# Optimization experiments

Measured on AMD Instinct MI355X. Metric: run time of the kernel, lower is better.

## Reference

```python
import jax, jax.numpy as jnp
import numpy as np

T, D, N, K, V = 4, 1024, 256, 64, 32000
SGLD_A, SGLD_B, SGLD_C = 0.01, 1.0, 0.55
PHI_VAR, ETA_VAR = 1.0, 1.0
ZERO = 1e-6

def jax_exp(x):
    return jnp.clip(jnp.exp(jnp.clip(x, -700.0, 700.0)), ZERO)

def setup_inputs() -> dict:
    key = jax.random.key(0)
    ks = jax.random.split(key, 13)
    W = jax.random.randint(ks[0], (T, D, N), 0, V, dtype=jnp.int32)
    Z = jax.random.randint(ks[1], (T, D, N), 0, K - 1, dtype=jnp.int32)
    prop_word_idx = jax.random.randint(ks[2], (T, D, N), 0, N, dtype=jnp.int32)
    prop_topic = jax.random.randint(ks[3], (T, D, N), 0, K - 1, dtype=jnp.int32)
    u_mh = jax.random.uniform(ks[4], (T, D, N, 2), dtype=jnp.float32)
    noise_eta = jax.random.normal(ks[5], (T, D), dtype=jnp.float32)
    noise_phi = jax.random.normal(ks[6], (T,), dtype=jnp.float32)
    alpha = jax.random.normal(ks[7], (T, K), dtype=jnp.float32)
    phi = jax.random.normal(ks[8], (T, V, K), dtype=jnp.float32) * 0.1
    eta = jax.random.normal(ks[9], (T, D, K), dtype=jnp.float32) * 0.1
    CDK = jax.random.uniform(ks[10], (T, D, K), dtype=jnp.float32) * (N / K)
    CWK = jax.random.uniform(ks[11], (T, V, K), dtype=jnp.float32)
    CK = jax.random.uniform(ks[12], (T, K), dtype=jnp.float32) * (D * N / K)
    return dict(W=W, Z=Z, prop_word_idx=prop_word_idx, prop_topic=prop_topic,
                u_mh=u_mh, noise_eta=noise_eta, noise_phi=noise_phi,
                alpha=alpha, phi=phi, eta=eta, CDK=CDK, CWK=CWK, CK=CK)

def reference(W, Z, prop_word_idx, prop_topic, u_mh, noise_eta, noise_phi,
              alpha, phi, eta, CDK, CWK, CK):
    eps = SGLD_A * (SGLD_B + 0.0) ** (-SGLD_C)  # SGLD step at iteration 0

    # --- SGLD update of eta (per doc), vmapped over (T, D) via broadcasting ---
    prior_eta = (alpha[:, None, :] - eta) / ETA_VAR                 # [T,D,K]
    grad_eta = CDK - N * jax.nn.softmax(eta, axis=-1)               # [T,D,K]
    eta_new = eta + eps / 2 * (grad_eta + prior_eta) + noise_eta[..., None] * eps

    tt = jnp.arange(T)[:, None, None]   # [T,1,1]
    dd = jnp.arange(D)[None, :, None]   # [1,D,1]

    # --- MH step 1: word-proposal (acceptance via phi ratio) ---
    pre = Z                                                           # [T,D,N]
    prop1 = jnp.take_along_axis(Z, prop_word_idx, axis=2)             # [T,D,N]
    a1 = jax_exp(phi[tt, W, prop1]) / jax_exp(phi[tt, W, pre])
    k1 = jnp.where(u_mh[..., 0] < a1, prop1, pre)

    # --- MH step 2: topic-proposal (acceptance via eta ratio) ---
    a2 = jax_exp(eta_new[tt, dd, prop_topic]) / jax_exp(eta_new[tt, dd, k1])
    z_new = jnp.where(u_mh[..., 1] < a2, prop_topic, k1)              # [T,D,N]

    # --- scatter counter updates (add new assignment, remove old) ---
    CDK_new = CDK.at[tt, dd, z_new].add(1.0).at[tt, dd, Z].add(-1.0)
    CWK_new = CWK.at[tt, W, z_new].add(1.0).at[tt, W, Z].add(-1.0)
    CK_new = CK.at[tt, z_new].add(1.0).at[tt, Z].add(-1.0)

    # --- SGLD update of phi: sequential over T (reads updated phi[t-1]) ---
    rows = [phi[t] for t in range(T)]   # each [V,K]
    phi_sigma = 1.0 / (1.0 / 100.0 + 1.0 / PHI_VAR)
    for t in range(T):
        if t == 0:
            prior = (2.0 * phi[1] * (phi_sigma / PHI_VAR) - 2.0 * rows[0]) / PHI_VAR
        elif t == T - 1:
            prior = (rows[t - 1] - rows[t]) / PHI_VAR
        else:
            prior = (phi[t + 1] + rows[t - 1] - 2.0 * rows[t]) / PHI_VAR
        grad = CWK_new[t] - CK_new[t][None, :] * jax.nn.softmax(rows[t], axis=0)
        rows[t] = rows[t] + eps / 2 * (grad + prior) + noise_phi[t] * eps
    phi_new = jnp.stack(rows)

    return (eta_new, phi_new, CDK_new, CWK_new, CK_new, z_new)
```

## Files before the change

kernel.cpp:

```cpp
#include <hip/hip_runtime.h>

#define T 4
#define D 1024
#define NN 256
#define K 64
#define V 32000
#define VK (V*K)
#define TD (T*D)

__device__ __forceinline__ float jexp(float x) {
    x = fminf(fmaxf(x, -700.0f), 700.0f);
    return fmaxf(expf(x), 1e-6f);
}


__global__ void phi_colsum_kernel(const float* __restrict__ phi,
                                  float* __restrict__ S_part,
                                  unsigned int* __restrict__ delta,
                                  const float* __restrict__ CK,
                                  float* __restrict__ CK_new)
{
    int blk = blockIdx.x;
    int tid = threadIdx.x;

    {
        uint4* dz = (uint4*)delta;
        int g = blk * 256 + tid;
        uint4 z4 = make_uint4(0u, 0u, 0u, 0u);
        #pragma unroll
        for (int i = 0; i < 8; ++i)
            dz[g + i * 128000] = z4;
    }
    if (blk == 0) CK_new[tid] = CK[tid];

    int t = blk / 125;
    int vbase = (blk % 125) * 256;
    int k = tid & 63;
    int r = tid >> 6;
    const float* base = phi + (size_t)t * VK;
    float s = 0.0f;
    #pragma unroll 4
    for (int it = 0; it < 64; ++it) {
        int v = vbase + it * 4 + r;
        s += expf(base[v * K + k]);
    }
    __shared__ float sm[256];
    sm[tid] = s;
    __syncthreads();
    if (tid < 64) {
        S_part[blk * 64 + tid] = sm[tid] + sm[tid + 64] +
                                 sm[tid + 128] + sm[tid + 192];
    }
}

__global__ void mh_eta_kernel(const int* __restrict__ W, const int* __restrict__ Z,
                              const int* __restrict__ pwi, const int* __restrict__ ptop,
                              const float* __restrict__ u, const float* __restrict__ phi,
                              const float* __restrict__ eta,
                              const float* __restrict__ alpha,
                              const float* __restrict__ noise_eta,
                              const float* __restrict__ CDK,
                              float* __restrict__ eta_new,
                              float* __restrict__ CDK_new,
                              unsigned int* __restrict__ plus,
                              unsigned int* __restrict__ minus,
                              float* __restrict__ z_out)
{
    int b = blockIdx.x;
    int r = ((b & 7) << 9) | (b >> 3);
    int t = r >> 10;
    int n = threadIdx.x;

    __shared__ float esh[K];
    __shared__ int   hist[K];

    int w     = W[r * NN + n];
    int pre   = Z[r * NN + n];
    int pw    = pwi[r * NN + n];
    int prop1 = Z[r * NN + pw];
    int pt    = ptop[r * NN + n];
    float2 uu = ((const float2*)u)[(size_t)r * NN + n];

    const float* prow = phi + ((size_t)t * V + w) * K;
    float f1 = prow[prop1];
    float f0 = prow[pre];

    float cdk = 0.0f;
    if (n < 64) {
        float x = eta[r * K + n];
        float m = x;
        #pragma unroll
        for (int off = 32; off >= 1; off >>= 1)
            m = fmaxf(m, __shfl_xor(m, off, 64));
        float e = expf(x - m);
        float s = e;
        #pragma unroll
        for (int off = 32; off >= 1; off >>= 1)
            s += __shfl_xor(s, off, 64);
        float smx = e / s;
        cdk = CDK[r * K + n];
        float grad  = cdk - (float)NN * smx;
        float prior = alpha[t * K + n] - x;
        float en = x + 0.005f * (grad + prior) + noise_eta[r] * 0.01f;
        esh[n] = en;
        eta_new[r * K + n] = en;
    } else if (n < 128) {
        hist[n - 64] = 0;
    }
    __syncthreads();

    float a1 = jexp(f1) / jexp(f0);
    int k1 = (uu.x < a1) ? prop1 : pre;

    float a2 = jexp(esh[pt]) / jexp(esh[k1]);
    int z = (uu.y < a2) ? pt : k1;

    atomicAdd(&hist[z], 1);
    atomicAdd(&hist[pre], -1);
    __syncthreads();

    z_out[r * NN + n] = (float)z;
    if (z != pre) {
        size_t rowbase = ((size_t)t * V + w) * 16;
        atomicAdd(&plus [rowbase + (z   >> 2)], 1u << ((z   & 3) * 8));
        atomicAdd(&minus[rowbase + (pre >> 2)], 1u << ((pre & 3) * 8));
    }
    if (n < K) {
        CDK_new[r * K + n] = cdk + (float)hist[n];
    }
}

__global__ void reduce_kernel(const float* __restrict__ S_part,
                              const float* __restrict__ CDKn,
                              const float* __restrict__ CDK,
                              float* __restrict__ S,
                              float* __restrict__ CK_new)
{
    int b = blockIdx.x;
    int tid = threadIdx.x;

    if (b < 4 && tid < 64) {
        float s = 0.0f;
        #pragma unroll 5
        for (int i = 0; i < 125; ++i)
            s += S_part[(b * 125 + i) * 64 + tid];
        S[b * 64 + tid] = s;
    }

    int t  = b >> 4;
    int k  = tid & 63;
    int dl = tid >> 6;
    int dbase = (b & 15) << 6;
    float s = 0.0f;
    #pragma unroll
    for (int i = 0; i < 16; ++i) {
        int d = dbase + dl + (i << 2);
        size_t idx = ((size_t)(t << 10) + d) * 64 + k;
        s += CDKn[idx] - CDK[idx];
    }
    __shared__ float sm[256];
    sm[tid] = s;
    __syncthreads();
    if (tid < 64) {
        float tot = sm[k] + sm[k + 64] + sm[k + 128] + sm[k + 192];
        if (tot != 0.0f) atomicAdd(&CK_new[(t << 6) + k], tot);
    }
}

__global__ void phi_update_kernel(const float* __restrict__ phi,
                                  const float* __restrict__ CWK,
                                  const unsigned int* __restrict__ plus,
                                  const unsigned int* __restrict__ minus,
                                  const float* __restrict__ CKn,
                                  const float* __restrict__ S,
                                  const float* __restrict__ noise_phi,
                                  float* __restrict__ phi_new,
                                  float* __restrict__ CWK_new)
{
    int i4 = blockIdx.x * 256 + threadIdx.x;
    int kg = i4 & 15;
    const float eps = 0.01f;
    const float half_eps = 0.005f;
    const float sig = 1.0f / 1.01f;

    const float4* phi4  = (const float4*)phi;
    const float4* cwk4  = (const float4*)CWK;
    const float4* ck4   = (const float4*)CKn;
    const float4* s4    = (const float4*)S;
    float4*       out4  = (float4*)phi_new;
    float4*       cwkn4 = (float4*)CWK_new;

    float4 p0 = phi4[i4];
    float4 p1 = phi4[i4 +     512000];
    float4 p2 = phi4[i4 + 2 * 512000];
    float4 p3 = phi4[i4 + 3 * 512000];

    float4 c0 = cwk4[i4];
    float4 c1 = cwk4[i4 +     512000];
    float4 c2 = cwk4[i4 + 2 * 512000];
    float4 c3 = cwk4[i4 + 3 * 512000];

    unsigned int pl0 = plus [i4],               mi0 = minus[i4];
    unsigned int pl1 = plus [i4 +     512000],  mi1 = minus[i4 +     512000];
    unsigned int pl2 = plus [i4 + 2 * 512000],  mi2 = minus[i4 + 2 * 512000];
    unsigned int pl3 = plus [i4 + 3 * 512000],  mi3 = minus[i4 + 3 * 512000];

    float4 ckn0 = ck4[kg],      ckn1 = ck4[16 + kg];
    float4 ckn2 = ck4[32 + kg], ckn3 = ck4[48 + kg];
    float4 ss0 = s4[kg],        ss1 = s4[16 + kg];
    float4 ss2 = s4[32 + kg],   ss3 = s4[48 + kg];

    float np0 = noise_phi[0] * eps, np1 = noise_phi[1] * eps;
    float np2 = noise_phi[2] * eps, np3 = noise_phi[3] * eps;

    float4 o0, o1, o2, o3, w0, w1, w2, w3;
    #pragma unroll
    for (int j = 0; j < 4; ++j) {
        int sh = j * 8;
        float q0 = (&p0.x)[j], q1 = (&p1.x)[j], q2 = (&p2.x)[j], q3 = (&p3.x)[j];
        float d0 = (float)((pl0 >> sh) & 255u) - (float)((mi0 >> sh) & 255u);
        float d1 = (float)((pl1 >> sh) & 255u) - (float)((mi1 >> sh) & 255u);
        float d2 = (float)((pl2 >> sh) & 255u) - (float)((mi2 >> sh) & 255u);
        float d3 = (float)((pl3 >> sh) & 255u) - (float)((mi3 >> sh) & 255u);
        float cw0 = (&c0.x)[j] + d0;
        float cw1 = (&c1.x)[j] + d1;
        float cw2 = (&c2.x)[j] + d2;
        float cw3 = (&c3.x)[j] + d3;
        (&w0.x)[j] = cw0; (&w1.x)[j] = cw1; (&w2.x)[j] = cw2; (&w3.x)[j] = cw3;

        float g0 = cw0 - (&ckn0.x)[j] * (expf(q0) / (&ss0.x)[j]);
        float g1 = cw1 - (&ckn1.x)[j] * (expf(q1) / (&ss1.x)[j]);
        float g2 = cw2 - (&ckn2.x)[j] * (expf(q2) / (&ss2.x)[j]);
        float g3 = cw3 - (&ckn3.x)[j] * (expf(q3) / (&ss3.x)[j]);

        float r0 = q0 + half_eps * (g0 + 2.0f * q1 * sig - 2.0f * q0) + np0;
        float r1 = q1 + half_eps * (g1 + q2 + r0 - 2.0f * q1)         + np1;
        float r2 = q2 + half_eps * (g2 + q3 + r1 - 2.0f * q2)         + np2;
        float r3 = q3 + half_eps * (g3 + r2 - q3)                      + np3;

        (&o0.x)[j] = r0; (&o1.x)[j] = r1; (&o2.x)[j] = r2; (&o3.x)[j] = r3;
    }

    out4[i4]              = o0;
    out4[i4 +     512000] = o1;
    out4[i4 + 2 * 512000] = o2;
    out4[i4 + 3 * 512000] = o3;

    cwkn4[i4]              = w0;
    cwkn4[i4 +     512000] = w1;
    cwkn4[i4 + 2 * 512000] = w2;
    cwkn4[i4 + 3 * 512000] = w3;
}

extern "C" void kernel_launch(void* const* d_in, const int* in_sizes, int n_in,
                              void* d_out, int out_size, void* d_ws, size_t ws_size,
                              hipStream_t stream)
{
    const int*   W         = (const int*)  d_in[0];
    const int*   Z         = (const int*)  d_in[1];
    const int*   pwi       = (const int*)  d_in[2];
    const int*   ptop      = (const int*)  d_in[3];
    const float* u_mh      = (const float*)d_in[4];
    const float* noise_eta = (const float*)d_in[5];
    const float* noise_phi = (const float*)d_in[6];
    const float* alpha     = (const float*)d_in[7];
    const float* phi       = (const float*)d_in[8];
    const float* eta       = (const float*)d_in[9];
    const float* CDK       = (const float*)d_in[10];
    const float* CWK       = (const float*)d_in[11];
    const float* CK        = (const float*)d_in[12];

    float* out     = (float*)d_out;
    float* eta_new = out;
    float* phi_new = out + 262144;
    float* CDK_new = out + 8454144;
    float* CWK_new = out + 8716288;
    float* CK_new  = out + 16908288;
    float* z_out   = out + 16908544;

    float* ws      = (float*)d_ws;
    float* S       = ws;
    float* S_part  = ws + 256;
    unsigned int* plus  = (unsigned int*)(ws + 256 + 32000);
    unsigned int* minus = plus + 2048000;

    phi_colsum_kernel<<<T * 125, 256, 0, stream>>>(phi, S_part, plus, CK, CK_new);
    mh_eta_kernel<<<TD, 256, 0, stream>>>(W, Z, pwi, ptop, u_mh, phi,
                                          eta, alpha, noise_eta, CDK,
                                          eta_new, CDK_new, plus, minus, z_out);
    reduce_kernel<<<64, 256, 0, stream>>>(S_part, CDK_new, CDK, S, CK_new);
    phi_update_kernel<<<VK / 1024, 256, 0, stream>>>(phi, CWK, plus, minus,
                                                     CK_new, S, noise_phi,
                                                     phi_new, CWK_new);
}
```

Baseline: 270.7 us.

## Fuse phi column-sum into MH/eta kernel and zero delta buffers via memset

```diff
diff --git a/kernel.cpp b/kernel.cpp
--- a/kernel.cpp
+++ b/kernel.cpp
@@ -14,66 +14,55 @@
 }
 
 
-__global__ void phi_colsum_kernel(const float* __restrict__ phi,
-                                  float* __restrict__ S_part,
-                                  unsigned int* __restrict__ delta,
-                                  const float* __restrict__ CK,
-                                  float* __restrict__ CK_new)
+__global__ void fused_kernel(const int* __restrict__ W, const int* __restrict__ Z,
+                             const int* __restrict__ pwi, const int* __restrict__ ptop,
+                             const float* __restrict__ u, const float* __restrict__ phi,
+                             const float* __restrict__ eta,
+                             const float* __restrict__ alpha,
+                             const float* __restrict__ noise_eta,
+                             const float* __restrict__ CDK,
+                             const float* __restrict__ CK,
+                             float* __restrict__ S_part,
+                             float* __restrict__ CK_new,
+                             float* __restrict__ eta_new,
+                             float* __restrict__ CDK_new,
+                             unsigned int* __restrict__ plus,
+                             unsigned int* __restrict__ minus,
+                             float* __restrict__ z_out)
 {
     int blk = blockIdx.x;
-    int tid = threadIdx.x;
-
-    {
-        uint4* dz = (uint4*)delta;
-        int g = blk * 256 + tid;
-        uint4 z4 = make_uint4(0u, 0u, 0u, 0u);
-        #pragma unroll
-        for (int i = 0; i < 8; ++i)
-            dz[g + i * 128000] = z4;
-    }
-    if (blk == 0) CK_new[tid] = CK[tid];
-
-    int t = blk / 125;
-    int vbase = (blk % 125) * 256;
-    int k = tid & 63;
-    int r = tid >> 6;
-    const float* base = phi + (size_t)t * VK;
-    float s = 0.0f;
-    #pragma unroll 4
-    for (int it = 0; it < 64; ++it) {
-        int v = vbase + it * 4 + r;
-        s += expf(base[v * K + k]);
-    }
+    int n = threadIdx.x;
+
     __shared__ float sm[256];
-    sm[tid] = s;
-    __syncthreads();
-    if (tid < 64) {
-        S_part[blk * 64 + tid] = sm[tid] + sm[tid + 64] +
-                                 sm[tid + 128] + sm[tid + 192];
-    }
-}
-
-__global__ void mh_eta_kernel(const int* __restrict__ W, const int* __restrict__ Z,
-                              const int* __restrict__ pwi, const int* __restrict__ ptop,
-                              const float* __restrict__ u, const float* __restrict__ phi,
-                              const float* __restrict__ eta,
-                              const float* __restrict__ alpha,
-                              const float* __restrict__ noise_eta,
-                              const float* __restrict__ CDK,
-                              float* __restrict__ eta_new,
-                              float* __restrict__ CDK_new,
-                              unsigned int* __restrict__ plus,
-                              unsigned int* __restrict__ minus,
-                              float* __restrict__ z_out)
-{
-    int b = blockIdx.x;
+    __shared__ float esh[K];
+    __shared__ int   hist[K];
+
+    if (blk < 500) {
+        if (blk == 0) CK_new[n] = CK[n];
+        int t = blk / 125;
+        int vbase = (blk % 125) * 256;
+        int k = n & 63;
+        int rr = n >> 6;
+        const float* base = phi + (size_t)t * VK;
+        float s = 0.0f;
+        #pragma unroll 4
+        for (int it = 0; it < 64; ++it) {
+            int v = vbase + it * 4 + rr;
+            s += expf(base[v * K + k]);
+        }
+        sm[n] = s;
+        __syncthreads();
+        if (n < 64) {
+            S_part[blk * 64 + n] = sm[n] + sm[n + 64] +
+                                   sm[n + 128] + sm[n + 192];
+        }
+        return;
+    }
+
+    int b = blk - 500;
     int r = ((b & 7) << 9) | (b >> 3);
     int t = r >> 10;
-    int n = threadIdx.x;
-
-    __shared__ float esh[K];
-    __shared__ int   hist[K];
-
+;
     int w     = W[r * NN + n];
     int pre   = Z[r * NN + n];
     int pw    = pwi[r * NN + n];
@@ -284,10 +273,12 @@
     unsigned int* plus  = (unsigned int*)(ws + 256 + 32000);
     unsigned int* minus = plus + 2048000;
 
-    phi_colsum_kernel<<<T * 125, 256, 0, stream>>>(phi, S_part, plus, CK, CK_new);
-    mh_eta_kernel<<<TD, 256, 0, stream>>>(W, Z, pwi, ptop, u_mh, phi,
-                                          eta, alpha, noise_eta, CDK,
-                                          eta_new, CDK_new, plus, minus, z_out);
+    hipMemsetAsync(plus, 0, 2 * (size_t)VK * sizeof(unsigned int) / 1, stream) ;
+
+    fused_kernel<<<500 + TD, 256, 0, stream>>>(W, Z, pwi, ptop, u_mh, phi,
+                                               eta, alpha, noise_eta, CDK, CK,
+                                               S_part, CK_new,
+                                               eta_new, CDK_new, plus, minus, z_out);
     reduce_kernel<<<64, 256, 0, stream>>>(S_part, CDK_new, CDK, S, CK_new);
     phi_update_kernel<<<VK / 1024, 256, 0, stream>>>(phi, CWK, plus, minus,
                                                      CK_new, S, noise_phi,
```

After: 265.1 us. 2.0% less time.
